# Optimization experiments

Measured on AMD Instinct MI355X. Metric: run time of the kernel, lower is better.

## Reference

```python
import jax, jax.numpy as jnp
import numpy as np
from math import factorial

# ---- static sizes from S2ConvNet_original ----
B_IN, B1, B2 = 30, 10, 6   # bandwidths: input S2 grid, after conv1 (SO3), after conv2 (SO3)
F1, F2, FOUT = 20, 40, 10
BATCH = 128


def _wigner_d(l, beta):
    """Wigner small-d matrix d^l_{m',m}(beta); rows m'=-l..l, cols m=-l..l."""
    cb, sb = np.cos(beta / 2.0), np.sin(beta / 2.0)
    d = np.zeros((2 * l + 1, 2 * l + 1))
    for i, mp in enumerate(range(-l, l + 1)):
        for j, m in enumerate(range(-l, l + 1)):
            pref = np.sqrt(float(factorial(l + mp) * factorial(l - mp) * factorial(l + m) * factorial(l - m)))
            acc = 0.0
            for s in range(max(0, m - mp), min(l + m, l - mp) + 1):
                den = factorial(l + m - s) * factorial(s) * factorial(mp - m + s) * factorial(l - mp - s)
                acc += ((-1.0) ** (mp - m + s) / den) * cb ** (2 * l + m - mp - 2 * s) * sb ** (mp - m + 2 * s)
            d[i, j] = pref * acc
    return d


def _dh_quad(b):
    """Driscoll-Healy beta grid / weights: sum_j w_j g(beta_j) ~ int_0^pi g(b) sin(b) db."""
    j = np.arange(2 * b)
    beta = np.pi * (2 * j + 1) / (4 * b)
    k = np.arange(b)[:, None]
    w = (2.0 / b) * np.sin(beta) * np.sum(np.sin((2 * k + 1) * beta[None, :]) / (2 * k + 1), axis=0)
    return beta, w


def _s2_grid(max_beta=np.pi / 8, n_alpha=8, n_beta=3):
    beta = np.arange(1, n_beta + 1) * max_beta / n_beta
    alpha = np.linspace(0, 2 * np.pi, n_alpha, endpoint=False)
    Bm, Am = np.meshgrid(beta, alpha, indexing='ij')
    return np.stack([Bm.ravel(), Am.ravel()], 1)  # [24, 2]


def _so3_grid(max_beta=np.pi / 8, max_gamma=2 * np.pi, n_alpha=8, n_beta=3, n_gamma=8):
    beta = np.arange(1, n_beta + 1) * max_beta / n_beta
    alpha = np.linspace(0, 2 * np.pi, n_alpha, endpoint=False)
    pre_gamma = np.linspace(0, max_gamma, n_gamma, endpoint=False)
    Bm, Am, Cm = np.meshgrid(beta, alpha, pre_gamma, indexing='ij')
    return np.stack([Bm.ravel(), Am.ravel(), (Cm - Am).ravel()], 1)  # [192, 3]


# ---------- conv1: S2 analysis (b 30 -> 10) ----------
_beta30, _qw30 = _dh_quad(B_IN)
_A1 = np.concatenate(
    [np.stack([_wigner_d(l, bb)[:, l] for bb in _beta30])  # d^l_{m,0}(beta_j): [60, 2l+1]
     * (_qw30 * (2 * np.pi / (2 * B_IN)))[:, None]
     for l in range(B1)], axis=1)  # [60, 100]
_A1J = jnp.asarray(_A1.astype(np.float32))
_M1 = np.concatenate([np.arange(-l, l + 1) for l in range(B1)])
_M1_IDX = np.mod(_M1, 2 * B_IN)

_g1 = _s2_grid()
_Y1 = np.concatenate(
    [np.stack([_wigner_d(l, bb)[:, l] for bb in _g1[:, 0]])
     * np.exp(-1j * np.outer(_g1[:, 1], np.arange(-l, l + 1)))
     for l in range(B1)], axis=1)  # [24, 100] complex
_Y1J = jnp.asarray(_Y1.astype(np.complex64))
_SC1 = float(1.0 / np.sqrt(len(_g1) * 1 * (B1 ** 4) / (B_IN ** 2)))

# ---------- SO3 synthesis tables at b=10 ----------
_beta10, _qw10 = _dh_quad(B1)
_D1S = [jnp.asarray(((2 * l + 1) * np.stack([_wigner_d(l, bb) for bb in _beta10])).astype(np.float32)) for l in range(B1)]
_FM1 = [np.mod(np.arange(-l, l + 1), 2 * B1) for l in range(B1)]

# ---------- conv2: SO3 analysis (b 10 -> 6) ----------
_W3 = np.concatenate(
    [(np.stack([_wigner_d(l, bb) for bb in _beta10])  # [20, 2l+1, 2l+1]
      * (_qw10 * (2 * np.pi / (2 * B1)) ** 2)[:, None, None]).reshape(2 * B1, -1)
     for l in range(B2)], axis=1)  # [20, 286]
_W3J = jnp.asarray(_W3.astype(np.float32))
_M2 = np.concatenate([np.repeat(np.arange(-l, l + 1), 2 * l + 1) for l in range(B2)])
_N2 = np.concatenate([np.tile(np.arange(-l, l + 1), 2 * l + 1) for l in range(B2)])
_M2_IDX = np.mod(_M2, 2 * B1)
_N2_IDX = np.mod(_N2, 2 * B1)

_g2 = _so3_grid()
_Y2 = np.concatenate(
    [np.stack([_wigner_d(l, bb) for bb in _g2[:, 0]]).reshape(len(_g2), -1)
     * (np.exp(-1j * np.outer(_g2[:, 1], np.arange(-l, l + 1)))[:, :, None]
        * np.exp(-1j * np.outer(_g2[:, 2], np.arange(-l, l + 1)))[:, None, :]).reshape(len(_g2), -1)
     for l in range(B2)], axis=1)  # [192, 286] complex: D^l_{mn}(alpha,beta,gamma)
_Y2J = jnp.asarray(_Y2.astype(np.complex64))
_SC2 = float(1.0 / np.sqrt(len(_g2) * F1 * (B2 ** 3) / (B1 ** 3)))

# ---------- SO3 synthesis tables at b=6 + integration weights ----------
_beta6, _qw6 = _dh_quad(B2)
_D2S = [jnp.asarray(((2 * l + 1) * np.stack([_wigner_d(l, bb) for bb in _beta6])).astype(np.float32)) for l in range(B2)]
_FM2 = [np.mod(np.arange(-l, l + 1), 2 * B2) for l in range(B2)]
_W_INT = jnp.asarray((_qw6 * (2 * np.pi / (2 * B2)) ** 2).astype(np.float32))


def _forward(x, k1, bias1, k2, bias2, w_out, b_lin):
    Bn = x.shape[0]
    # ===== conv1: S2 correlation -> function on SO(3) at b=10 =====
    xf = jnp.fft.fft(x.astype(jnp.complex64), axis=-1)                 # FFT over alpha: [B,1,60,60]
    xhat = jnp.einsum('bfjs,js->sbf', xf[..., _M1_IDX], _A1J)          # [100,B,1] S2 spectrum
    k1h = jnp.einsum('iop,ps->sio', (k1 * _SC1).astype(jnp.complex64), _Y1J)  # [100,1,F1]
    Ffreq = jnp.zeros((Bn, F1, 2 * B1, 2 * B1, 2 * B1), jnp.complex64)  # [B,F1,beta,m,n]
    for l in range(B1):
        s0, s1 = l * l, (l + 1) * (l + 1)
        # z^l_{mn} = sum_fin xhat^l_m conj(khat^l_n)  (outer product per degree l)
        zl = jnp.einsum('mbi,nio->bmno', xhat[s0:s1], jnp.conj(k1h[s0:s1]))
        fb = jnp.einsum('bmno,jmn->bojmn', zl, _D1S[l])                # (2l+1) d^l_{mn}(beta_j)
        Ffreq = Ffreq.at[:, :, :, _FM1[l][:, None], _FM1[l][None, :]].add(fb)
    x1 = jnp.fft.ifft2(Ffreq, axes=(-2, -1)).real * float((2 * B1) ** 2)  # synth over alpha,gamma
    x1 = jax.nn.relu(x1 + bias1[None, :, None, None, None])            # [B,F1,20,20,20]
    # ===== conv2: SO(3) correlation -> b=6 =====
    x1f = jnp.fft.fft2(x1.astype(jnp.complex64), axes=(-2, -1))        # FFT over alpha,gamma
    xhat2 = jnp.einsum('bfjs,js->sbf', x1f[:, :, :, _M2_IDX, _N2_IDX], _W3J)  # [286,B,F1]
    k2h = jnp.einsum('iop,ps->sio', (k2 * _SC2).astype(jnp.complex64), _Y2J)  # [286,F1,F2]
    Ffreq2 = jnp.zeros((Bn, F2, 2 * B2, 2 * B2, 2 * B2), jnp.complex64)
    base = 0
    for l in range(B2):
        L = 2 * l + 1
        xl = xhat2[base:base + L * L].reshape(L, L, Bn, F1)            # [m,k,B,Fin]
        gl = jnp.conj(k2h[base:base + L * L].reshape(L, L, F1, F2))    # [n,k,Fin,Fout]
        zl = jnp.einsum('mkbi,nkio->bmno', xl, gl)                     # z^l = xhat^l ghat^l^H
        fb = jnp.einsum('bmno,jmn->bojmn', zl, _D2S[l])
        Ffreq2 = Ffreq2.at[:, :, :, _FM2[l][:, None], _FM2[l][None, :]].add(fb)
        base += L * L
    x2 = jnp.fft.ifft2(Ffreq2, axes=(-2, -1)).real * float((2 * B2) ** 2)
    x2 = jax.nn.relu(x2 + bias2[None, :, None, None, None])            # [B,F2,12,12,12]
    # ===== so3_integrate + linear head =====
    feat = jnp.einsum('bfjkp,j->bf', x2, _W_INT)                       # [B,F2]
    return feat @ w_out.T + b_lin


def setup_inputs() -> dict:
    key = jax.random.key(0)
    ks = jax.random.split(key, 4)
    return {
        'x': jax.random.normal(ks[0], (BATCH, 1, 2 * B_IN, 2 * B_IN), jnp.float32),
        'k1': jax.random.normal(ks[1], (1, F1, len(_g1)), jnp.float32),
        'bias1': jnp.zeros((F1,), jnp.float32),
        'k2': jax.random.normal(ks[2], (F1, F2, len(_g2)), jnp.float32),
        'bias2': jnp.zeros((F2,), jnp.float32),
        'w_out': jax.random.normal(ks[3], (FOUT, F2), jnp.float32) / np.sqrt(F2).astype(np.float32),
        'b_lin': jnp.zeros((FOUT,), jnp.float32),
    }


def reference(x, k1, bias1, k2, bias2, w_out, b_lin):
    return _forward(x, k1, bias1, k2, bias2, w_out, b_lin)
```

## Files before the change

### kernel.cpp

```cpp
#include <hip/hip_runtime.h>
#include <math.h>

#define PI_D 3.14159265358979323846

#define BATCH 128
#define F1 20
#define F2 40
#define FOUT 10
#define NS1 100
#define NS2 286
#define NH2 146

typedef float v2f __attribute__((ext_vector_type(2)));
#define PKFMA(a,b,c) __builtin_elementwise_fma((a),(b),(c))
#define SW(v) __builtin_shufflevector((v),(v),1,0)
static __device__ __forceinline__ v2f bc2(float s){ return (v2f){s,s}; }
static __device__ __forceinline__ v2f ldv(const float2* p){ return *(const v2f*)p; }

#define GLOAD_LDS16(g,l) __builtin_amdgcn_global_load_lds( \
  (const __attribute__((address_space(1))) void*)(g), \
  (__attribute__((address_space(3))) void*)(l), 16, 0, 0)

__constant__ int ZB10c[11] = {0,1,10,35,84,165,286,455,680,969,1330};
__constant__ int B2OFFc[7] = {0,1,10,35,84,165,286};
__constant__ int HOFFc[7]  = {0,1,6,19,44,85,146};
__constant__ float2 E8c[8] = {
  { 1.f, 0.f}, { 0.70710678118654752f,-0.70710678118654752f},
  { 0.f,-1.f}, {-0.70710678118654752f,-0.70710678118654752f},
  {-1.f, 0.f}, {-0.70710678118654752f, 0.70710678118654752f},
  { 0.f, 1.f}, { 0.70710678118654752f, 0.70710678118654752f}};

#define WFENCE do{ __builtin_amdgcn_sched_barrier(0); \
  asm volatile("s_waitcnt lgkmcnt(0)" ::: "memory"); \
  __builtin_amdgcn_sched_barrier(0); }while(0)

__device__ inline void h_decode(int h, int& l, int& m, int& n){
  l=0; while(HOFFc[l+1]<=h) ++l;
  int r=h-HOFFc[l], L=2*l+1;
  if(r<l+1){ n=0; m=r; }
  else { int q=r-(l+1); n=q/L+1; m=q%L-l; }
}

__device__ inline double ipow_d(double x, int n){ double r=1.0; for(int i=0;i<n;++i) r*=x; return r; }

__device__ double wigd_t(int l, int mp, int m, double beta, const double* F){
  double cb=cos(0.5*beta), sb=sin(0.5*beta);
  double pref=sqrt(F[l+mp]*F[l-mp]*F[l+m]*F[l-m]);
  int s0 = (m-mp>0) ? (m-mp) : 0;
  int s1 = (l+m < l-mp) ? (l+m) : (l-mp);
  double acc=0.0;
  for(int s=s0;s<=s1;++s){
    double den=F[l+m-s]*F[s]*F[mp-m+s]*F[l-mp-s];
    double t=ipow_d(cb,2*l+m-mp-2*s)*ipow_d(sb,mp-m+2*s)/den;
    acc += ((mp-m+s)&1)? -t : t;
  }
  return pref*acc;
}

__device__ double dhw(int b, int j){
  double beta=PI_D*(2*j+1)/(4.0*b);
  double s=0.0;
  for(int k=0;k<b;++k) s += sin((2*k+1)*beta)/(2*k+1);
  return (2.0/b)*sin(beta)*s;
}

__global__ void gen_all(const float* __restrict__ k2,
                        float* A1, float* D1SJ, float* W3H, float* D2SJ,
                        float* D3_2, float* D3_1, float* WINT,
                        float2* E60, float2* E20, float2* E12,
                        unsigned* zLUT, unsigned* xh2LUT, unsigned* h2LUT,
                        unsigned short* fhLUT, unsigned* aLUT,
                        float2* KA){
  __shared__ double factS[21];
  __shared__ double dhwS[60];
  __shared__ float2 E8L[8];
  int blk=blockIdx.x, t=threadIdx.x;
  if(t==0){ double f=1.0; factS[0]=1.0; for(int k=1;k<=20;++k){ f*=(double)k; factS[k]=f; } }
  if(blk<24){ if(t<60) dhwS[t]=dhw(30,t); }
  else if(blk>=76 && blk<82){ if(t<20) dhwS[t]=dhw(10,t); }
  if(t<8) E8L[t]=E8c[t];
  __syncthreads();
  const double* F=factS;
  if(blk<24){
    int idx=blk*256+t;
    if(idx<6000){
      int j=idx/NS1, s=idx%NS1;
      int l=0; while((l+1)*(l+1)<=s) ++l;
      int m=s-l*l-l;
      double beta=PI_D*(2*j+1)/120.0;
      A1[idx]=(float)(wigd_t(l,m,0,beta,F)*dhwS[j]*(2.0*PI_D/60.0));
    }
  } else if(blk<76){
    int idx=(blk-24)*256+t; if(idx>=13300) return;
    int j=idx/1330, s=idx%1330;
    int l=0; while(ZB10c[l+1]<=s) ++l;
    int r=s-ZB10c[l]; int L=2*l+1;
    int mi=r/L, ni=r%L;
    double beta=PI_D*(2*j+1)/40.0;
    float v=(float)((2*l+1)*wigd_t(l,mi-l,ni-l,beta,F));
    D1SJ[j*1330+s]=v;
    int s2=ZB10c[l]+(2*l-mi)*L+ni;
    D1SJ[(19-j)*1330+s2]=(ni&1)? -v : v;
  } else if(blk<82){
    int idx=(blk-76)*256+t;
    if(idx<10*NH2){
      int j=idx/NH2, h=idx%NH2;
      int l,m,n; h_decode(h,l,m,n);
      double beta=PI_D*(2*j+1)/40.0;
      double c=2.0*PI_D/20.0;
      float v=(float)(wigd_t(l,m,n,beta,F)*dhwS[j]*c*c);
      W3H[j*NH2+h]=v;
      if(n==0){
        W3H[(19-j)*NH2+h]=((l+m)&1)? -v : v;
      } else {
        int L=2*l+1;
        int hp=HOFFc[l]+(l+1)+(n-1)*L+(l-m);
        W3H[(19-j)*NH2+hp]=((l+n)&1)? -v : v;
      }
    }
  } else if(blk<89){
    int idx=(blk-82)*256+t; if(idx>=1716) return;
    int j=idx/286, s=idx%286;
    int l=0; while(B2OFFc[l+1]<=s) ++l;
    int r=s-B2OFFc[l]; int L=2*l+1;
    int mi=r/L, ni=r%L;
    double beta=PI_D*(2*j+1)/24.0;
    float v=(float)((2*l+1)*wigd_t(l,mi-l,ni-l,beta,F));
    D2SJ[j*286+s]=v;
    int s2=B2OFFc[l]+(2*l-mi)*L+ni;
    D2SJ[(11-j)*286+s2]=(ni&1)? -v : v;
  } else if(blk<93){
    int idx=(blk-89)*256+t; if(idx>=3*286) return;
    int bi=idx/286, s=idx%286;
    int l=0; while(B2OFFc[l+1]<=s) ++l;
    int r=s-B2OFFc[l]; int L=2*l+1;
    int mi=r/L, ni=r%L;
    double beta=(bi+1)*(PI_D/8.0)/3.0;
    D3_2[idx]=(float)wigd_t(l,mi-l,ni-l,beta,F);
  } else if(blk<95){
    int idx=(blk-93)*256+t; if(idx>=3*100) return;
    int bi=idx/100, s=idx%100;
    int l=0; while((l+1)*(l+1)<=s) ++l;
    int m=s-l*l-l;
    double beta=(bi+1)*(PI_D/8.0)/3.0;
    D3_1[idx]=(float)wigd_t(l,m,0,beta,F);
  } else if(blk==95){
    if(t<12){ double c=2.0*PI_D/12.0; WINT[t]=(float)(dhw(6,t)*c*c); }
    if(t<60){ double a=2.0*PI_D*t/60.0; E60[t]=make_float2((float)cos(a),(float)sin(a)); }
    if(t<20){ double a=2.0*PI_D*t/20.0; E20[t]=make_float2((float)cos(a),(float)sin(a)); }
    if(t<12){ double a=2.0*PI_D*t/12.0; E12[t]=make_float2((float)cos(a),(float)sin(a)); }
  } else if(blk<102){
    int idx=(blk-96)*256+t; if(idx>=1330) return;
    int l=0; while(ZB10c[l+1]<=idx) ++l;
    int r=idx-ZB10c[l], L=2*l+1;
    int mi=r/L, ni=r%L;
    unsigned s1x=(unsigned)(l*l+mi), s1k=(unsigned)(l*l+ni);
    zLUT[idx]=s1x|(s1k<<16);
  } else if(blk==102){
    if(t<146){
      int l,m,n; h_decode(t,l,m,n);
      int L=2*l+1;
      int s2 =B2OFFc[l]+(m+l)*L+(n+l);
      int s2p=B2OFFc[l]+(l-m)*L+(l-n);
      unsigned sg=(unsigned)((m+n)&1);
      xh2LUT[t]=(unsigned)s2 | ((unsigned)s2p<<10) | (sg<<20);
      h2LUT[t]=(unsigned)l | ((unsigned)(m+l)<<4) | ((unsigned)(n+l)<<8) | ((unsigned)s2<<12);
      fhLUT[t]=(unsigned short)((n==0)? m : 6+(n-1)*11+(m+5));
    }
  } else if(blk==103){
    if(t==0){
      int idx=0;
      for(int lm=0;lm<10;++lm){
        for(int m=0;m<10;++m){
          int nlo=(m==0)?0:-9;
          for(int n=nlo;n<10;++n){
            int an=n<0?-n:n;
            int lmin=m>an?m:an;
            if(lmin!=lm) continue;
            int L=2*lm+1;
            int zi=ZB10c[lm]+(m+lm)*L+(n+lm);
            aLUT[idx++]=(unsigned)zi | ((unsigned)m<<11) | ((unsigned)(n+9)<<15) | ((unsigned)lm<<20);
          }
        }
      }
    }
  } else {
    int idx=(blk-104)*256+t;
    if(idx<153600){
      int ai=idx&7, q=(idx>>3)&7;
      int r2=idx>>6;
      int bi=r2%3, io=r2/3;
      const float* kp=k2+(size_t)io*192+bi*64+ai*8;
      v2f acc={0.f,0.f};
      int ph=0;
      #pragma unroll
      for(int gi=0;gi<8;++gi){
        acc=PKFMA(bc2(kp[gi]), ldv(&E8L[ph]), acc);
        ph=(ph+q)&7;
      }
      KA[(size_t)io*192+bi*64+q*8+ai]=make_float2(acc.x,acc.y);
    }
  }
}

__global__ __launch_bounds__(256) void front_k(const float* __restrict__ x,
    const float* __restrict__ k1,
    const float2* __restrict__ E60, const float* __restrict__ A1,
    const float* __restrict__ D3_1,
    float2* __restrict__ XHAT, float2* __restrict__ K1H){
  int blk=blockIdx.x, t=threadIdx.x;
  if(blk<128){
    __shared__ __align__(16) float xs[3600];
    __shared__ float2 E60s[60];
    __shared__ float2 XFs[1140];
    if(t<60){ float2 e=E60[t]; E60s[t]=make_float2(e.x,-e.y); }
    {
      const float4* src=(const float4*)(x+blk*3600);
      float4* dst=(float4*)xs;
      for(int i=t;i<900;i+=256) GLOAD_LDS16(src+i, dst+(i&~63));
    }
    __syncthreads();
    for(int idx=t; idx<1140; idx+=256){
      int j=idx/19, mi=idx%19;
      int step=(mi<9)? mi+51 : mi-9;
      bool modd = ((mi&1)==0);
      const float* xr=xs+j*60;
      v2f acc={0.f,0.f};
      int k=0;
      for(int a=0;a<30;++a){
        float xv = modd ? (xr[a]-xr[a+30]) : (xr[a]+xr[a+30]);
        acc=PKFMA(bc2(xv), ldv(&E60s[k]), acc);
        k+=step; if(k>=60)k-=60;
      }
      XFs[idx]=make_float2(acc.x,acc.y);
    }
    __syncthreads();
    for(int s=t; s<100; s+=256){
      int l=0; while((l+1)*(l+1)<=s) ++l;
      int m=s-l*l-l;
      const float2* xf=&XFs[m+9];
      v2f acc={0.f,0.f};
      for(int j=0;j<60;++j){
        acc=PKFMA(bc2(A1[j*NS1+s]), ldv(&xf[j*19]), acc);
      }
      XHAT[blk*NS1+s]=make_float2(acc.x,acc.y);
    }
  } else {
    __shared__ float2 E8s[8];
    if(t<8) E8s[t]=E8c[t];
    __syncthreads();
    int idx=(blk-128)*256+t;
    if(idx<F1*NS1){
      int o=idx/NS1, s=idx%NS1;
      int l=0; while((l+1)*(l+1)<=s) ++l;
      int m=s-l*l-l;
      int mm=m&7;
      v2f acc={0.f,0.f};
      for(int bi=0;bi<3;++bi){
        v2f sum={0.f,0.f};
        int q=0;
        #pragma unroll
        for(int ai=0;ai<8;++ai){
          sum=PKFMA(bc2(k1[o*24+bi*8+ai]), ldv(&E8s[q]), sum);
          q=(q+mm)&7;
        }
        acc=PKFMA(bc2(D3_1[bi*100+s]), sum, acc);
      }
      const float SC1f = 0.06123724356957945f;
      K1H[idx]=make_float2(acc.x*SC1f, acc.y*SC1f);
    }
  }
}

__global__ __launch_bounds__(512,6) void fused1(
    const float2* __restrict__ XHAT, const float2* __restrict__ K1H,
    const float* __restrict__ D1SJ, const float* __restrict__ W3H,
    const float2* __restrict__ E20, const float* __restrict__ bias1,
    const unsigned* __restrict__ zLUT, const unsigned* __restrict__ xh2LUT,
    const unsigned short* __restrict__ fhLUT, const unsigned* __restrict__ aLUT,
    float2* __restrict__ XH2){
  const int b=blockIdx.x, o=blockIdx.y, t=threadIdx.x;
  const int ln=t&63, w=t>>6;
  __shared__ __align__(16) float2 zS[1330];
  __shared__ __align__(16) float2 TWE2[400];
  __shared__ __align__(16) float2 regA[8][200];
  __shared__ __align__(16) float2 regB[8][190];

  for(int idx=t; idx<400; idx+=512){
    int r=idx/20, c=idx%20;
    TWE2[idx]=E20[(r*c)%20];
  }
  {
    float2* st=regA[0];
    if(t<100) st[t]=XHAT[b*NS1+t];
    else if(t<200) st[t]=K1H[o*NS1+(t-100)];
  }
  __syncthreads();
  {
    const float2* st=regA[0];
    for(int idx=t; idx<1330; idx+=512){
      unsigned u=zLUT[idx];
      v2f xa=ldv(&st[u&0xffff]);
      v2f kb=ldv(&st[100+(u>>16)]);
      v2f p1=xa*kb, p2=xa*SW(kb);
      zS[idx]=make_float2(p1.x+p1.y, p2.y-p2.x);
    }
  }
  __syncthreads();

  const float bb1=bias1[o];
  float2* G  = regA[w];
  float*  vbF= (float*)regA[w];
  float2* Fq = regA[w];
  float*  RB = (float*)regB[w];
  float*  Sx = RB;
  float*  Sy = RB+180;
  float*  T0f= RB+360;
  float2* U_T= regB[w];
  v2f fa0={0.f,0.f}, fa1=fa0, fa2=fa0;

  const int BROW[19]={11,12,13,14,15,16,17,18,19,0,1,2,3,4,5,6,7,8,9};

  for(int jq=0;jq<3;++jq){
    const int j=jq*8+w;
    const bool act=(j<20);
    const float* Dg=D1SJ + (act? j*1330 : 0);
    if(act) for(int idx=ln; idx<181; idx+=64){
      unsigned au=aLUT[idx];
      int zi=au&2047;
      int m=(au>>11)&15, n9=(au>>15)&31, l=(au>>20)&15;
      int L=2*l+1;
      int m2=2*m+2;
      v2f a0={0.f,0.f};
      for(; l<10; ++l){
        a0=PKFMA(ldv(&zS[zi]), bc2(Dg[zi]), a0);
        zi += L*L + 2*L + m2; L += 2;
      }
      *(v2f*)&G[m*19+n9]=a0;
    }
    WFENCE;
    if(act){
    if(ln<45){
      int mb=ln/5+1, gp=(ln%5)*2;
      const float2* Gr=&G[mb*19];
      v2f E1a={0.f,0.f},E2a=E1a,O1a=E1a,O2a=E1a;
      v2f E1b=E1a,E2b=E1a,O1b=E1a,O2b=E1a;
      #pragma unroll
      for(int c=0;c<19;++c){
        v2f gv=ldv(&Gr[c]);
        const float* er=(const float*)&TWE2[BROW[c]*20+gp];
        float4 e01=*(const float4*)er;
        v2f e0={e01.x,e01.y}, e1={e01.z,e01.w};
        if(c&1){
          E1a=PKFMA(gv,e0,E1a); E2a=PKFMA(gv,SW(e0),E2a);
          E1b=PKFMA(gv,e1,E1b); E2b=PKFMA(gv,SW(e1),E2b);
        } else {
          O1a=PKFMA(gv,e0,O1a); O2a=PKFMA(gv,SW(e0),O2a);
          O1b=PKFMA(gv,e1,O1b); O2b=PKFMA(gv,SW(e1),O2b);
        }
      }
      int si=(mb-1)*20+gp;
      float exa=E1a.x-E1a.y, oxa=O1a.x-O1a.y;
      float eya=E2a.x+E2a.y, oya=O2a.x+O2a.y;
      float exb=E1b.x-E1b.y, oxb=O1b.x-O1b.y;
      float eyb=E2b.x+E2b.y, oyb=O2b.x+O2b.y;
      *(v2f*)&Sx[si]   =(v2f){2.f*(exa+oxa), 2.f*(exb+oxb)};
      *(v2f*)&Sx[si+10]=(v2f){2.f*(exa-oxa), 2.f*(exb-oxb)};
      *(v2f*)&Sy[si]   =(v2f){2.f*(eya+oya), 2.f*(eyb+oyb)};
      *(v2f*)&Sy[si+10]=(v2f){2.f*(eya-oya), 2.f*(eyb-oyb)};
    } else if(ln<50){
      int gt=(ln-45)*2;
      float g0x=G[9].x;
      float Ea=0.f,Eb=0.f,Oa=0.f,Ob=0.f;
      #pragma unroll
      for(int n=1;n<10;++n){
        float2 gv=G[9+n];
        const float* er=(const float*)&TWE2[n*20+gt];
        float4 e01=*(const float4*)er;
        float ra=gv.x*e01.x-gv.y*e01.y;
        float rb=gv.x*e01.z-gv.y*e01.w;
        if((n&1)==0){ Ea+=ra; Eb+=rb; } else { Oa+=ra; Ob+=rb; }
      }
      T0f[gt]   =g0x+2.f*(Ea+Oa);
      T0f[gt+1] =g0x+2.f*(Eb+Ob);
      T0f[gt+10]=g0x+2.f*(Ea-Oa);
      T0f[gt+11]=g0x+2.f*(Eb-Ob);
    }
    }
    WFENCE;
    if(act && ln<50){
      int a=ln/5, g0=(ln%5)*4;
      v2f i01={T0f[g0]+bb1, T0f[g0+1]+bb1};
      v2f i23={T0f[g0+2]+bb1, T0f[g0+3]+bb1};
      v2f P01={0.f,0.f},P23=P01,Q01=P01,Q23=P01;
      #pragma unroll
      for(int m=1;m<10;++m){
        float2 e=TWE2[a*20+m];
        v2f sx01=*(const v2f*)&Sx[(m-1)*20+g0];
        v2f sx23=*(const v2f*)&Sx[(m-1)*20+g0+2];
        v2f sy01=*(const v2f*)&Sy[(m-1)*20+g0];
        v2f sy23=*(const v2f*)&Sy[(m-1)*20+g0+2];
        if(m&1){
          Q01=PKFMA(bc2(e.x),sx01,Q01); Q01=PKFMA(bc2(-e.y),sy01,Q01);
          Q23=PKFMA(bc2(e.x),sx23,Q23); Q23=PKFMA(bc2(-e.y),sy23,Q23);
        } else {
          P01=PKFMA(bc2(e.x),sx01,P01); P01=PKFMA(bc2(-e.y),sy01,P01);
          P23=PKFMA(bc2(e.x),sx23,P23); P23=PKFMA(bc2(-e.y),sy23,P23);
        }
      }
      v2f z2={0.f,0.f};
      v2f vA01=i01+P01+Q01, vA23=i23+P23+Q23;
      v2f vB01=i01+P01-Q01, vB23=i23+P23-Q23;
      *(v2f*)&vbF[a*20+g0]       =__builtin_elementwise_max(vA01,z2);
      *(v2f*)&vbF[a*20+g0+2]     =__builtin_elementwise_max(vA23,z2);
      *(v2f*)&vbF[(a+10)*20+g0]  =__builtin_elementwise_max(vB01,z2);
      *(v2f*)&vbF[(a+10)*20+g0+2]=__builtin_elementwise_max(vB23,z2);
    }
    WFENCE;
    if(act && ln<60){
      int a=ln/3, np=ln%3;
      int nu0=2*np, nu1=2*np+1;
      int r0=(np==0)?0:(20-2*np);
      int r1=19-2*np;
      const float* vp=&vbF[a*20];
      const float2* T0r=&TWE2[r0*20];
      const float2* T1r=&TWE2[r1*20];
      v2f u0={0.f,0.f}, u1=u0;
      #pragma unroll
      for(int g=0;g<10;++g){
        float va=vp[g], vb=vp[g+10];
        u0=PKFMA(bc2(va+vb), ldv(&T0r[g]), u0);
        u1=PKFMA(bc2(va-vb), ldv(&T1r[g]), u1);
      }
      *(v2f*)&U_T[nu0*20+a]=u0; *(v2f*)&U_T[nu1*20+a]=u1;
    }
    WFENCE;
    if(act && ln<61){
      int mu,nu;
      if(ln<6){ mu=ln; nu=0; } else { int q=ln-6; nu=q/11+1; mu=q%11-5; }
      int mm=(mu+20)%20;
      int rm=(20-mm)%20;
      bool modd=(mm&1);
      const float2* Ur=&U_T[nu*20];
      const float2* Er=&TWE2[rm*20];
      v2f p1={0.f,0.f}, p2=p1;
      #pragma unroll
      for(int a=0;a<10;++a){
        v2f ua=ldv(&Ur[a]), ub=ldv(&Ur[a+10]);
        v2f u = modd ? (ua-ub) : (ua+ub);
        v2f e=ldv(&Er[a]);
        p1=PKFMA(u,e,p1);
        p2=PKFMA(u,SW(e),p2);
      }
      Fq[ln]=make_float2(p1.x-p1.y, p2.x+p2.y);
    }
    WFENCE;
    if(act){
      const float* W3r=W3H + j*NH2;
      fa0=PKFMA(bc2(W3r[ln]),    ldv(&Fq[fhLUT[ln]]),    fa0);
      fa1=PKFMA(bc2(W3r[64+ln]), ldv(&Fq[fhLUT[64+ln]]), fa1);
      if(ln<18) fa2=PKFMA(bc2(W3r[128+ln]), ldv(&Fq[fhLUT[128+ln]]), fa2);
    }
    WFENCE;
  }
  regB[w][ln]=make_float2(fa0.x,fa0.y);
  regB[w][64+ln]=make_float2(fa1.x,fa1.y);
  if(ln<18) regB[w][128+ln]=make_float2(fa2.x,fa2.y);
  __syncthreads();
  for(int h=t; h<146; h+=512){
    unsigned u=xh2LUT[h];
    int s2=u&1023, s2p=(u>>10)&1023;
    float sg=((u>>20)&1)? -1.f : 1.f;
    float2 a0=regB[0][h], a1=regB[1][h], a2=regB[2][h], a3=regB[3][h];
    float2 a4=regB[4][h], a5=regB[5][h], a6=regB[6][h], a7=regB[7][h];
    float2 a=make_float2(a0.x+a1.x+a2.x+a3.x+a4.x+a5.x+a6.x+a7.x,
                         a0.y+a1.y+a2.y+a3.y+a4.y+a5.y+a6.y+a7.y);
    XH2[(b*286+s2 )*F1+o]=a;
    XH2[(b*286+s2p)*F1+o]=make_float2(sg*a.x, -sg*a.y);
  }
}

__global__ __launch_bounds__(192) void k2h_k(const float2* __restrict__ KA,
                      const float* __restrict__ D3_2,
                      const unsigned* __restrict__ h2LUT, const unsigned* __restrict__ xh2LUT,
                      float2* __restrict__ K2H){
  __shared__ float2 kaS[192];
  __shared__ float2 E8s[8];
  int io=blockIdx.x, t=threadIdx.x;
  int i=io/F2, o=io%F2;
  if(t<8) E8s[t]=E8c[t];
  kaS[t]=KA[(size_t)io*192+t];
  __syncthreads();
  if(t>=146) return;
  unsigned hu=h2LUT[t];
  int l=hu&15, mi=(hu>>4)&15, ni=(hu>>8)&15, s2=hu>>12;
  int m=mi-l, n=ni-l;
  unsigned xu=xh2LUT[t];
  int s2p=(xu>>10)&1023;
  float sg=((xu>>20)&1)? -1.f : 1.f;
  int q=n&7, p=(m-n)&7;
  v2f a1={0.f,0.f}, a2=a1;
  for(int bi=0;bi<3;++bi){
    const float2* kp=&kaS[bi*64+q*8];
    v2f s1={0.f,0.f}, s2v=s1;
    int ph=0;
    #pragma unroll
    for(int ai=0;ai<8;++ai){
      v2f ka=ldv(&kp[ai]), e=ldv(&E8s[ph]);
      s1=PKFMA(ka,e,s1); s2v=PKFMA(ka,SW(e),s2v);
      ph=(ph+p)&7;
    }
    v2f dv=bc2(D3_2[bi*286+s2]);
    a1=PKFMA(dv,s1,a1); a2=PKFMA(dv,s2v,a2);
  }
  const float SC2f = 0.034722222222222224f;
  float re=(a1.x-a1.y)*SC2f, im=(a2.x+a2.y)*SC2f;
  K2H[((size_t)o*286+s2)*F1+i]=make_float2(re,im);
  K2H[((size_t)o*286+s2p)*F1+i]=make_float2(sg*re,-sg*im);
}

__global__ __launch_bounds__(256,3) void fused2(
    const float2* __restrict__ XH2, const float2* __restrict__ K2H,
    const float* __restrict__ D2SJ, const float* __restrict__ WINT,
    const float2* __restrict__ E12, const float* __restrict__ bias2,
    const unsigned* __restrict__ h2LUT, const unsigned* __restrict__ xh2LUT,
    float* __restrict__ FEAT){
  const int b=blockIdx.x, o=blockIdx.y, t=threadIdx.x;
  const int ln=t&63, w=t>>6;
  __shared__ __align__(16) float2 Xs[2420];
  __shared__ __align__(16) float2 Ks[2420];
  __shared__ float2 zpS[1144];
  __shared__ float2 z2S[286];
  __shared__ float  redS[256];
  float2* alias=(float2*)Xs;
  float2* TWE12=alias;

  const int gb[4]={0,84,165,286};
  const int hb[4]={0,44,85,146};
  for(int grp=0; grp<3; ++grp){
    int row0=gb[grp], rows=gb[grp+1]-row0;
    {
      int cnt4=rows*10;
      const float4* xsrc=(const float4*)(XH2+(size_t)(b*286+row0)*F1);
      const float4* ksrc=(const float4*)(K2H+(size_t)(o*286+row0)*F1);
      float4* xd=(float4*)Xs; float4* kd=(float4*)Ks;
      for(int i4=t;i4<cnt4;i4+=256){
        int wb=i4&~63;
        GLOAD_LDS16(xsrc+i4, xd+wb);
        GLOAD_LDS16(ksrc+i4, kd+wb);
      }
    }
    __syncthreads();
    int nh=hb[grp+1]-hb[grp];
    for(int idx=t; idx<4*nh; idx+=256){
      int hl=idx>>2, iq=idx&3;
      int h=hb[grp]+hl;
      unsigned hu=h2LUT[h];
      int l=hu&15, mi=(hu>>4)&15, ni=(hu>>8)&15, s2=hu>>12;
      int L=2*l+1;
      int xr0=(B2OFFc[l]-row0)+mi*L;
      int kr0=(B2OFFc[l]-row0)+ni*L;
      v2f p1={0.f,0.f}, p2=p1;
      for(int k=0;k<L;++k){
        const float2* xp=Xs+(xr0+k)*F1+iq*5;
        const float2* kp=Ks+(kr0+k)*F1+iq*5;
        #pragma unroll
        for(int i=0;i<5;++i){
          v2f xa=ldv(&xp[i]), kb=ldv(&kp[i]);
          p1=PKFMA(xa,kb,p1);
          p2=PKFMA(xa,SW(kb),p2);
        }
      }
      zpS[iq*286+s2]=make_float2(p1.x+p1.y, p2.y-p2.x);
    }
    __syncthreads();
  }
  for(int idx=t; idx<146; idx+=256){
    unsigned xu=xh2LUT[idx];
    int s2=xu&1023, s2p=(xu>>10)&1023;
    float sg=((xu>>20)&1)? -1.f : 1.f;
    float2 a;
    a.x=zpS[0*286+s2].x+zpS[1*286+s2].x+zpS[2*286+s2].x+zpS[3*286+s2].x;
    a.y=zpS[0*286+s2].y+zpS[1*286+s2].y+zpS[2*286+s2].y+zpS[3*286+s2].y;
    z2S[s2]=a;
    z2S[s2p]=make_float2(sg*a.x,-sg*a.y);
  }
  __syncthreads();
  for(int idx=t; idx<144; idx+=256){
    int r=idx/12, c=idx%12;
    TWE12[idx]=E12[(r*c)%12];
  }
  __syncthreads();

  float2* base2=alias+144+w*400;
  float2* G2_0=base2; float2* G2_1=base2+66; float2* G2_2=base2+132;
  float*  SP=(float*)(base2+198);
  float*  S2x0=SP, *S2x1=SP+60, *S2x2=SP+120;
  float*  S2y0=SP+180, *S2y1=SP+240, *S2y2=SP+300;
  float*  T02=SP+360;
  float personal=0.f;
  const float b2v=bias2[o];
  const int j0=3*w, j1=3*w+1, j2=3*w+2;
  const float* Dg0=D2SJ + j0*286;
  const float* Dg1=D2SJ + j1*286;
  const float* Dg2=D2SJ + j2*286;
  const int BR12[11]={7,8,9,10,11,0,1,2,3,4,5};

  if(ln<61){
    int m,n;
    if(ln<6){m=0;n=ln;} else {int qq=ln-6;m=qq/11+1;n=qq%11-5;}
    int an=n<0?-n:n; int l=m>an?m:an; int L=2*l+1;
    int zi=B2OFFc[l]+(m+l)*L+(n+l); int m2=2*m+2;
    v2f a0={0.f,0.f}, a1=a0, a2=a0;
    for(;l<6;++l){
      v2f zv=ldv(&z2S[zi]);
      a0=PKFMA(zv, bc2(Dg0[zi]), a0);
      a1=PKFMA(zv, bc2(Dg1[zi]), a1);
      a2=PKFMA(zv, bc2(Dg2[zi]), a2);
      zi+=L*L+2*L+m2; L+=2;
    }
    int gi=m*11+(n+5);
    *(v2f*)&G2_0[gi]=a0; *(v2f*)&G2_1[gi]=a1; *(v2f*)&G2_2[gi]=a2;
  }
  WFENCE;
  if(ln<30){
    int m=ln/6+1, g=ln%6;
    v2f E1_0={0.f,0.f},E2_0=E1_0,O1_0=E1_0,O2_0=E1_0;
    v2f E1_1=E1_0,E2_1=E1_0,O1_1=E1_0,O2_1=E1_0;
    v2f E1_2=E1_0,E2_2=E1_0,O1_2=E1_0,O2_2=E1_0;
    #pragma unroll
    for(int c=0;c<11;++c){
      float2 ef=TWE12[BR12[c]*12+g];
      v2f e={ef.x,ef.y};
      v2f g0=ldv(&G2_0[m*11+c]), g1=ldv(&G2_1[m*11+c]), g2=ldv(&G2_2[m*11+c]);
      if(c&1){
        E1_0=PKFMA(g0,e,E1_0); E2_0=PKFMA(g0,SW(e),E2_0);
        E1_1=PKFMA(g1,e,E1_1); E2_1=PKFMA(g1,SW(e),E2_1);
        E1_2=PKFMA(g2,e,E1_2); E2_2=PKFMA(g2,SW(e),E2_2);
      } else {
        O1_0=PKFMA(g0,e,O1_0); O2_0=PKFMA(g0,SW(e),O2_0);
        O1_1=PKFMA(g1,e,O1_1); O2_1=PKFMA(g1,SW(e),O2_1);
        O1_2=PKFMA(g2,e,O1_2); O2_2=PKFMA(g2,SW(e),O2_2);
      }
    }
    int si=(m-1)*12+g;
    {
      float Ex=E1_0.x-E1_0.y, Ox=O1_0.x-O1_0.y;
      float Ey=E2_0.x+E2_0.y, Oy=O2_0.x+O2_0.y;
      S2x0[si]=2.f*(Ex+Ox); S2x0[si+6]=2.f*(Ex-Ox);
      S2y0[si]=2.f*(Ey+Oy); S2y0[si+6]=2.f*(Ey-Oy);
    }
    {
      float Ex=E1_1.x-E1_1.y, Ox=O1_1.x-O1_1.y;
      float Ey=E2_1.x+E2_1.y, Oy=O2_1.x+O2_1.y;
      S2x1[si]=2.f*(Ex+Ox); S2x1[si+6]=2.f*(Ex-Ox);
      S2y1[si]=2.f*(Ey+Oy); S2y1[si+6]=2.f*(Ey-Oy);
    }
    {
      float Ex=E1_2.x-E1_2.y, Ox=O1_2.x-O1_2.y;
      float Ey=E2_2.x+E2_2.y, Oy=O2_2.x+O2_2.y;
      S2x2[si]=2.f*(Ex+Ox); S2x2[si+6]=2.f*(Ex-Ox);
      S2y2[si]=2.f*(Ey+Oy); S2y2[si+6]=2.f*(Ey-Oy);
    }
  } else if(ln<42){
    int g=ln-30;
    float r0=G2_0[5].x, r1=G2_1[5].x, r2=G2_2[5].x;
    #pragma unroll
    for(int n=1;n<6;++n){
      float2 e=TWE12[n*12+g];
      float2 g0=G2_0[5+n], g1=G2_1[5+n], g2=G2_2[5+n];
      r0+=2.f*(g0.x*e.x-g0.y*e.y);
      r1+=2.f*(g1.x*e.x-g1.y*e.y);
      r2+=2.f*(g2.x*e.x-g2.y*e.y);
    }
    T02[g]=r0; T02[12+g]=r1; T02[24+g]=r2;
  }
  WFENCE;
  if(ln<36){
    float w0=WINT[j0], w1=WINT[j1], w2=WINT[j2];
    int a=ln/3, g4=(ln%3)*4;
    v2f iA0={T02[g4]+b2v, T02[g4+1]+b2v},       iB0={T02[g4+2]+b2v, T02[g4+3]+b2v};
    v2f iA1={T02[12+g4]+b2v, T02[12+g4+1]+b2v}, iB1={T02[12+g4+2]+b2v, T02[12+g4+3]+b2v};
    v2f iA2={T02[24+g4]+b2v, T02[24+g4+1]+b2v}, iB2={T02[24+g4+2]+b2v, T02[24+g4+3]+b2v};
    #pragma unroll
    for(int m=1;m<6;++m){
      float2 e=TWE12[a*12+m];
      v2f ex=bc2(e.x), eny=bc2(-e.y);
      int si=(m-1)*12+g4;
      v2f sx, sy;
      sx=*(const v2f*)&S2x0[si];   sy=*(const v2f*)&S2y0[si];
      iA0=PKFMA(ex,sx,iA0); iA0=PKFMA(eny,sy,iA0);
      sx=*(const v2f*)&S2x0[si+2]; sy=*(const v2f*)&S2y0[si+2];
      iB0=PKFMA(ex,sx,iB0); iB0=PKFMA(eny,sy,iB0);
      sx=*(const v2f*)&S2x1[si];   sy=*(const v2f*)&S2y1[si];
      iA1=PKFMA(ex,sx,iA1); iA1=PKFMA(eny,sy,iA1);
      sx=*(const v2f*)&S2x1[si+2]; sy=*(const v2f*)&S2y1[si+2];
      iB1=PKFMA(ex,sx,iB1); iB1=PKFMA(eny,sy,iB1);
      sx=*(const v2f*)&S2x2[si];   sy=*(const v2f*)&S2y2[si];
      iA2=PKFMA(ex,sx,iA2); iA2=PKFMA(eny,sy,iA2);
      sx=*(const v2f*)&S2x2[si+2]; sy=*(const v2f*)&S2y2[si+2];
      iB2=PKFMA(ex,sx,iB2); iB2=PKFMA(eny,sy,iB2);
    }
    v2f z2={0.f,0.f};
    v2f rA0=__builtin_elementwise_max(iA0,z2), rB0=__builtin_elementwise_max(iB0,z2);
    v2f rA1=__builtin_elementwise_max(iA1,z2), rB1=__builtin_elementwise_max(iB1,z2);
    v2f rA2=__builtin_elementwise_max(iA2,z2), rB2=__builtin_elementwise_max(iB2,z2);
    personal += w0*(rA0.x+rA0.y+rB0.x+rB0.y)
              + w1*(rA1.x+rA1.y+rB1.x+rB1.y)
              + w2*(rA2.x+rA2.y+rB2.x+rB2.y);
  }
  redS[t]=personal;
  __syncthreads();
  for(int s=128;s>0;s>>=1){
    if(t<s) redS[t]+=redS[t+s];
    __syncthreads();
  }
  if(t==0) FEAT[b*F2+o]=redS[0];
}

__global__ void head_k(const float* __restrict__ FEAT, const float* __restrict__ w_out,
                       const float* __restrict__ b_lin, float* __restrict__ out){
  int idx=blockIdx.x*blockDim.x+threadIdx.x;
  if(idx>=BATCH*FOUT) return;
  int b=idx/FOUT, q=idx%FOUT;
  float acc=b_lin[q];
  for(int f=0;f<F2;++f) acc += FEAT[b*F2+f]*w_out[q*F2+f];
  out[idx]=acc;
}

extern "C" void kernel_launch(void* const* d_in, const int* in_sizes, int n_in,
                              void* d_out, int out_size, void* d_ws, size_t ws_size,
                              hipStream_t stream) {
  const float* x    =(const float*)d_in[0];
  const float* k1   =(const float*)d_in[1];
  const float* bias1=(const float*)d_in[2];
  const float* k2   =(const float*)d_in[3];
  const float* bias2=(const float*)d_in[4];
  const float* w_out=(const float*)d_in[5];
  const float* b_lin=(const float*)d_in[6];
  float* out=(float*)d_out;

  char* ws=(char*)d_ws;
  float*  A1   =(float* )(ws+0);
  float*  D1SJ =(float* )(ws+24000);
  float*  W3H  =(float* )(ws+130400);
  float*  D2SJ =(float* )(ws+142080);
  float*  D3_2 =(float* )(ws+155808);
  float*  D3_1 =(float* )(ws+159248);
  float*  WINT =(float* )(ws+160448);
  float2* E60  =(float2*)(ws+160496);
  float2* E20  =(float2*)(ws+160976);
  float2* E12  =(float2*)(ws+161136);
  unsigned* zLUT=(unsigned*)(ws+161248);
  unsigned* xh2LUT=(unsigned*)(ws+166576);
  unsigned* h2LUT =(unsigned*)(ws+167160);
  unsigned short* fhLUT=(unsigned short*)(ws+167744);
  unsigned* aLUT =(unsigned*)(ws+168048);
  float2* XHAT =(float2*)(ws+168784);
  float2* K1H  =(float2*)(ws+271184);
  float2* KA   =(float2*)(ws+287184);
  float2* XH2  =(float2*)(ws+1515984);
  float2* K2H  =(float2*)(ws+7373264);
  float*  FEAT =(float* )(ws+9203664);

  (void)in_sizes; (void)n_in; (void)out_size; (void)ws_size;

  gen_all<<<704,256,0,stream>>>(k2,A1,D1SJ,W3H,D2SJ,D3_2,D3_1,WINT,E60,E20,E12,
                                zLUT,xh2LUT,h2LUT,fhLUT,aLUT,KA);
  front_k<<<136,256,0,stream>>>(x,k1,E60,A1,D3_1,XHAT,K1H);
  dim3 g1(BATCH,F1);
  fused1<<<g1,512,0,stream>>>(XHAT,K1H,D1SJ,W3H,E20,bias1,zLUT,xh2LUT,fhLUT,aLUT,XH2);
  k2h_k<<<F1*F2,192,0,stream>>>(KA,D3_2,h2LUT,xh2LUT,K2H);
  dim3 g2(BATCH,F2);
  fused2<<<g2,256,0,stream>>>(XH2,K2H,D2SJ,WINT,E12,bias2,h2LUT,xh2LUT,FEAT);
  head_k<<<(BATCH*FOUT+255)/256,256,0,stream>>>(FEAT,w_out,b_lin,out);
}
```

Before: 202.7 us.

## Fold k2h kernel into front_k and shrink fused2 shared memory

The separate k2h_k launch becomes 800 extra blocks appended to front_k, which removes one kernel launch and its serialization gap. In fused2, the partial-sum buffer is indexed by half-index h instead of s2, cutting it from 1144 to 584 entries. z2S and redS now alias the Xs/Ks buffers, and one __syncthreads is dropped. The lower LDS footprint may let more blocks of fused2 be resident per CU. The risk is that the aliased regions overlap live data when the barrier is removed (z2S is written into Xs while TWE12 is also written into Xs).

```diff
diff --git a/kernel.cpp b/kernel.cpp
--- a/kernel.cpp
+++ b/kernel.cpp
@@ -204,10 +204,12 @@
 }
 
 __global__ __launch_bounds__(256) void front_k(const float* __restrict__ x,
-    const float* __restrict__ k1,
+    const float* __restrict__ k1, const float2* __restrict__ KA,
+    const float* __restrict__ D3_2,
     const float2* __restrict__ E60, const float* __restrict__ A1,
     const float* __restrict__ D3_1,
-    float2* __restrict__ XHAT, float2* __restrict__ K1H){
+    const unsigned* __restrict__ h2LUT, const unsigned* __restrict__ xh2LUT,
+    float2* __restrict__ XHAT, float2* __restrict__ K1H, float2* __restrict__ K2H){
   int blk=blockIdx.x, t=threadIdx.x;
   if(blk<128){
     __shared__ __align__(16) float xs[3600];
@@ -245,7 +247,7 @@
       }
       XHAT[blk*NS1+s]=make_float2(acc.x,acc.y);
     }
-  } else {
+  } else if(blk<136){
     __shared__ float2 E8s[8];
     if(t<8) E8s[t]=E8c[t];
     __syncthreads();
@@ -269,6 +271,40 @@
       const float SC1f = 0.06123724356957945f;
       K1H[idx]=make_float2(acc.x*SC1f, acc.y*SC1f);
     }
+  } else {
+    __shared__ float2 kaS[192];
+    __shared__ float2 E8k[8];
+    int io=blk-136;
+    int i=io/F2, o=io%F2;
+    if(t<8) E8k[t]=E8c[t];
+    if(t<192) kaS[t]=KA[(size_t)io*192+t];
+    __syncthreads();
+    if(t>=146) return;
+    unsigned hu=h2LUT[t];
+    int l=hu&15, mi=(hu>>4)&15, ni=(hu>>8)&15, s2=hu>>12;
+    int m=mi-l, n=ni-l;
+    unsigned xu=xh2LUT[t];
+    int s2p=(xu>>10)&1023;
+    float sg=((xu>>20)&1)? -1.f : 1.f;
+    int q=n&7, p=(m-n)&7;
+    v2f a1={0.f,0.f}, a2=a1;
+    for(int bi=0;bi<3;++bi){
+      const float2* kp=&kaS[bi*64+q*8];
+      v2f s1={0.f,0.f}, s2v=s1;
+      int ph=0;
+      #pragma unroll
+      for(int ai=0;ai<8;++ai){
+        v2f ka=ldv(&kp[ai]), e=ldv(&E8k[ph]);
+        s1=PKFMA(ka,e,s1); s2v=PKFMA(ka,SW(e),s2v);
+        ph=(ph+p)&7;
+      }
+      v2f dv=bc2(D3_2[bi*286+s2]);
+      a1=PKFMA(dv,s1,a1); a2=PKFMA(dv,s2v,a2);
+    }
+    const float SC2f = 0.034722222222222224f;
+    float re=(a1.x-a1.y)*SC2f, im=(a2.x+a2.y)*SC2f;
+    K2H[((size_t)o*286+s2)*F1+i]=make_float2(re,im);
+    K2H[((size_t)o*286+s2p)*F1+i]=make_float2(sg*re,-sg*im);
   }
 }
 
@@ -480,45 +516,6 @@
   }
 }
 
-__global__ __launch_bounds__(192) void k2h_k(const float2* __restrict__ KA,
-                      const float* __restrict__ D3_2,
-                      const unsigned* __restrict__ h2LUT, const unsigned* __restrict__ xh2LUT,
-                      float2* __restrict__ K2H){
-  __shared__ float2 kaS[192];
-  __shared__ float2 E8s[8];
-  int io=blockIdx.x, t=threadIdx.x;
-  int i=io/F2, o=io%F2;
-  if(t<8) E8s[t]=E8c[t];
-  kaS[t]=KA[(size_t)io*192+t];
-  __syncthreads();
-  if(t>=146) return;
-  unsigned hu=h2LUT[t];
-  int l=hu&15, mi=(hu>>4)&15, ni=(hu>>8)&15, s2=hu>>12;
-  int m=mi-l, n=ni-l;
-  unsigned xu=xh2LUT[t];
-  int s2p=(xu>>10)&1023;
-  float sg=((xu>>20)&1)? -1.f : 1.f;
-  int q=n&7, p=(m-n)&7;
-  v2f a1={0.f,0.f}, a2=a1;
-  for(int bi=0;bi<3;++bi){
-    const float2* kp=&kaS[bi*64+q*8];
-    v2f s1={0.f,0.f}, s2v=s1;
-    int ph=0;
-    #pragma unroll
-    for(int ai=0;ai<8;++ai){
-      v2f ka=ldv(&kp[ai]), e=ldv(&E8s[ph]);
-      s1=PKFMA(ka,e,s1); s2v=PKFMA(ka,SW(e),s2v);
-      ph=(ph+p)&7;
-    }
-    v2f dv=bc2(D3_2[bi*286+s2]);
-    a1=PKFMA(dv,s1,a1); a2=PKFMA(dv,s2v,a2);
-  }
-  const float SC2f = 0.034722222222222224f;
-  float re=(a1.x-a1.y)*SC2f, im=(a2.x+a2.y)*SC2f;
-  K2H[((size_t)o*286+s2)*F1+i]=make_float2(re,im);
-  K2H[((size_t)o*286+s2p)*F1+i]=make_float2(sg*re,-sg*im);
-}
-
 __global__ __launch_bounds__(256,3) void fused2(
     const float2* __restrict__ XH2, const float2* __restrict__ K2H,
     const float* __restrict__ D2SJ, const float* __restrict__ WINT,
@@ -529,11 +526,11 @@
   const int ln=t&63, w=t>>6;
   __shared__ __align__(16) float2 Xs[2420];
   __shared__ __align__(16) float2 Ks[2420];
-  __shared__ float2 zpS[1144];
-  __shared__ float2 z2S[286];
-  __shared__ float  redS[256];
+  __shared__ float2 zpS[584];
   float2* alias=(float2*)Xs;
   float2* TWE12=alias;
+  float2* z2S  =alias+1744;
+  float*  redS =(float*)Ks;
 
   const int gb[4]={0,84,165,286};
   const int hb[4]={0,44,85,146};
@@ -556,7 +553,7 @@
       int hl=idx>>2, iq=idx&3;
       int h=hb[grp]+hl;
       unsigned hu=h2LUT[h];
-      int l=hu&15, mi=(hu>>4)&15, ni=(hu>>8)&15, s2=hu>>12;
+      int l=hu&15, mi=(hu>>4)&15, ni=(hu>>8)&15;
       int L=2*l+1;
       int xr0=(B2OFFc[l]-row0)+mi*L;
       int kr0=(B2OFFc[l]-row0)+ni*L;
@@ -571,7 +568,7 @@
           p2=PKFMA(xa,SW(kb),p2);
         }
       }
-      zpS[iq*286+s2]=make_float2(p1.x+p1.y, p2.y-p2.x);
+      zpS[iq*146+h]=make_float2(p1.x+p1.y, p2.y-p2.x);
     }
     __syncthreads();
   }
@@ -580,12 +577,11 @@
     int s2=xu&1023, s2p=(xu>>10)&1023;
     float sg=((xu>>20)&1)? -1.f : 1.f;
     float2 a;
-    a.x=zpS[0*286+s2].x+zpS[1*286+s2].x+zpS[2*286+s2].x+zpS[3*286+s2].x;
-    a.y=zpS[0*286+s2].y+zpS[1*286+s2].y+zpS[2*286+s2].y+zpS[3*286+s2].y;
+    a.x=zpS[idx].x+zpS[146+idx].x+zpS[292+idx].x+zpS[438+idx].x;
+    a.y=zpS[idx].y+zpS[146+idx].y+zpS[292+idx].y+zpS[438+idx].y;
     z2S[s2]=a;
     z2S[s2p]=make_float2(sg*a.x,-sg*a.y);
   }
-  __syncthreads();
   for(int idx=t; idx<144; idx+=256){
     int r=idx/12, c=idx%12;
     TWE12[idx]=E12[(r*c)%12];
@@ -767,10 +763,9 @@
 
   gen_all<<<704,256,0,stream>>>(k2,A1,D1SJ,W3H,D2SJ,D3_2,D3_1,WINT,E60,E20,E12,
                                 zLUT,xh2LUT,h2LUT,fhLUT,aLUT,KA);
-  front_k<<<136,256,0,stream>>>(x,k1,E60,A1,D3_1,XHAT,K1H);
+  front_k<<<936,256,0,stream>>>(x,k1,KA,D3_2,E60,A1,D3_1,h2LUT,xh2LUT,XHAT,K1H,K2H);
   dim3 g1(BATCH,F1);
   fused1<<<g1,512,0,stream>>>(XHAT,K1H,D1SJ,W3H,E20,bias1,zLUT,xh2LUT,fhLUT,aLUT,XH2);
-  k2h_k<<<F1*F2,192,0,stream>>>(KA,D3_2,h2LUT,xh2LUT,K2H);
   dim3 g2(BATCH,F2);
   fused2<<<g2,256,0,stream>>>(XH2,K2H,D2SJ,WINT,E12,bias2,h2LUT,xh2LUT,FEAT);
   head_k<<<(BATCH*FOUT+255)/256,256,0,stream>>>(FEAT,w_out,b_lin,out);
```

After: 198.2 us. 2.2% less time.
